# Optimization experiments

Measured on AMD Instinct MI355X. Metric: run time of the kernel, lower is better.

The kernel has to match this reference:

```python
import jax, jax.numpy as jnp
import numpy as np


def _rotate_half(x):
    half = x.shape[-1] // 2
    x1, x2 = x[..., :half], x[..., half:]
    return jnp.concatenate([-x2, x1], axis=-1)


def setup_inputs() -> dict:
    key = jax.random.key(0)
    ks = jax.random.split(key, 7)
    B, T, D, H, Hd = 4, 2048, 1024, 16, 64
    x = jax.random.normal(ks[0], (B, T, D), dtype=jnp.float32)
    # RoPE tables (realistic: built from inv freqs)
    inv_freq = 1.0 / (10000.0 ** (jnp.arange(0, Hd, 2, dtype=jnp.float32) / Hd))
    pos = jnp.arange(T, dtype=jnp.float32)
    freqs = pos[:, None] * inv_freq[None, :]            # (T, Hd/2)
    emb = jnp.concatenate([freqs, freqs], axis=-1)       # (T, Hd)
    cos, sin = jnp.cos(emb), jnp.sin(emb)
    s = 1.0 / np.sqrt(D)
    w_q = jax.random.normal(ks[1], (D, D), dtype=jnp.float32) * s
    w_k = jax.random.normal(ks[2], (D, D), dtype=jnp.float32) * s
    w_v = jax.random.normal(ks[3], (D, D), dtype=jnp.float32) * s
    w_o = jax.random.normal(ks[4], (D, D), dtype=jnp.float32) * s
    return {"x": x, "cos": cos, "sin": sin, "w_q": w_q, "w_k": w_k, "w_v": w_v, "w_o": w_o}


def reference(x, cos, sin, w_q, w_k, w_v, w_o):
    B, T, D = x.shape
    H = 16
    Hd = D // H
    scale = Hd ** -0.5
    # nn.Linear(bias=False): y = x @ W.T
    q = (x @ w_q.T).reshape(B, T, H, Hd).transpose(0, 2, 1, 3)  # (B,H,T,Hd)
    k = (x @ w_k.T).reshape(B, T, H, Hd).transpose(0, 2, 1, 3)
    v = (x @ w_v.T).reshape(B, T, H, Hd).transpose(0, 2, 1, 3)
    c = cos[None, None, :, :]
    s = sin[None, None, :, :]
    q = q * c + _rotate_half(q) * s
    k = k * c + _rotate_half(k) * s
    scores = jnp.einsum('bhqd,bhkd->bhqk', q, k) * scale  # (B,H,T,T)
    causal = jnp.tril(jnp.ones((T, T), dtype=bool))
    scores = jnp.where(causal[None, None], scores, -jnp.inf)
    weights = jax.nn.softmax(scores, axis=-1)
    out = jnp.einsum('bhqk,bhkd->bhqd', weights, v)
    out = out.transpose(0, 2, 1, 3).reshape(B, T, D)
    return out @ w_o.T
```

## Files before the change

kernel.cpp:

```cpp
#include <hip/hip_runtime.h>
#include <stdint.h>

typedef __attribute__((ext_vector_type(8))) __bf16 bf16x8;
typedef __attribute__((ext_vector_type(4))) float floatx4;


__device__ __forceinline__ unsigned short f2bf(float f) {
    unsigned int u = __float_as_uint(f);
    u += 0x7FFFu + ((u >> 16) & 1u);
    return (unsigned short)(u >> 16);
}
__device__ __forceinline__ unsigned int pack2bf(float lo, float hi) {
    return (unsigned int)f2bf(lo) | ((unsigned int)f2bf(hi) << 16);
}
__device__ __forceinline__ unsigned int packtrunc(float lo, float hi) {
    return __builtin_amdgcn_perm(__float_as_uint(hi), __float_as_uint(lo), 0x07060302u);
}

__device__ __forceinline__ void gl_lds16(const void* g, void* l) {
    __builtin_amdgcn_global_load_lds(
        (const __attribute__((address_space(1))) void*)g,
        (__attribute__((address_space(3))) void*)l, 16, 0, 0);
}


__global__ void cvt_all(const float* __restrict__ x,  const float* __restrict__ wq,
                        const float* __restrict__ wk, const float* __restrict__ wv,
                        const float* __restrict__ wo,
                        unsigned short* __restrict__ xb,  unsigned short* __restrict__ wqb,
                        unsigned short* __restrict__ wkb, unsigned short* __restrict__ wvb,
                        unsigned short* __restrict__ wob) {
    int i = blockIdx.x * blockDim.x + threadIdx.x;
    const float* in; unsigned short* out; int idx;
    if (i < 2097152) { in = x; out = xb; idx = i; }
    else {
        int j = i - 2097152; int wsel = j >> 18; idx = j & 262143;
        in  = (wsel == 0) ? wq  : (wsel == 1) ? wk  : (wsel == 2) ? wv  : wo;
        out = (wsel == 0) ? wqb : (wsel == 1) ? wkb : (wsel == 2) ? wvb : wob;
    }
    float4 v = ((const float4*)in)[idx];
    ushort4 o;
    o.x = f2bf(v.x); o.y = f2bf(v.y); o.z = f2bf(v.z); o.w = f2bf(v.w);
    ((ushort4*)out)[idx] = o;
}

__global__ __launch_bounds__(256, 2)
void gemm_qkv(const unsigned short* __restrict__ A,
              const unsigned short* __restrict__ Wq,
              const unsigned short* __restrict__ Wk,
              const unsigned short* __restrict__ Wv,
              const float* __restrict__ cosp,
              const float* __restrict__ sinp,
              unsigned short* __restrict__ outq,
              unsigned short* __restrict__ outk,
              unsigned short* __restrict__ outvt)
{
    constexpr int K = 1024;
    __shared__ __align__(16) unsigned short As[128 * 32];
    __shared__ __align__(16) unsigned short Bs[128 * 32];

    const int t    = threadIdx.x;
    const int w    = t >> 6;
    const int lane = t & 63;
    const int c    = lane & 15;
    const int quad = lane >> 4;
    const int wr   = w >> 1, wc = w & 1;

    const int m0    = blockIdx.x * 128;
    const int which = blockIdx.y >> 3;
    const int n0    = (blockIdx.y & 7) * 128;
    const unsigned short* W = (which == 0) ? Wq : (which == 1) ? Wk : Wv;
    const bool vmode = (which == 2);

    const int srow = t >> 2;
    const int scol = (t & 3) * 8;
    const unsigned short* ga0 = A + (size_t)(m0 + srow) * K + scol;
    const unsigned short* ga1 = A + (size_t)(m0 + srow + 64) * K + scol;
    const unsigned short* gb0 = W + (size_t)(n0 + srow) * K + scol;
    const unsigned short* gb1 = W + (size_t)(n0 + srow + 64) * K + scol;
    void* lA0 = (char*)As + t * 16;
    void* lA1 = (char*)As + 4096 + t * 16;
    void* lB0 = (char*)Bs + t * 16;
    void* lB1 = (char*)Bs + 4096 + t * 16;

    floatx4 acc[4][4] = {};

    const int arow = wr * 64;
    const int brow = wc * 64;

    for (int k0 = 0; k0 < K; k0 += 32) {
        __syncthreads();
        gl_lds16(ga0 + k0, lA0);
        gl_lds16(ga1 + k0, lA1);
        gl_lds16(gb0 + k0, lB0);
        gl_lds16(gb1 + k0, lB1);
        __syncthreads();
        bf16x8 af[4], bfr[4];
        #pragma unroll
        for (int mi = 0; mi < 4; mi++)
            af[mi] = *(const bf16x8*)&As[(arow + mi * 16 + c) * 32 + quad * 8];
        #pragma unroll
        for (int ni = 0; ni < 4; ni++)
            bfr[ni] = *(const bf16x8*)&Bs[(brow + ni * 16 + c) * 32 + quad * 8];
        if (vmode) {
            #pragma unroll
            for (int mi = 0; mi < 4; mi++)
                #pragma unroll
                for (int ni = 0; ni < 4; ni++)
                    acc[mi][ni] = __builtin_amdgcn_mfma_f32_16x16x32_bf16(
                        af[mi], bfr[ni], acc[mi][ni], 0, 0, 0);
        } else {
            #pragma unroll
            for (int mi = 0; mi < 4; mi++)
                #pragma unroll
                for (int ni = 0; ni < 4; ni++)
                    acc[mi][ni] = __builtin_amdgcn_mfma_f32_16x16x32_bf16(
                        bfr[ni], af[mi], acc[mi][ni], 0, 0, 0);
        }
    }

    const int hh = (n0 + wc * 64) >> 6;
    if (vmode) {
        #pragma unroll
        for (int mi = 0; mi < 4; mi++) {
            int t0 = m0 + wr * 64 + mi * 16 + quad * 4;
            int b = t0 >> 11, tt0 = t0 & 2047;
            #pragma unroll
            for (int ni = 0; ni < 4; ni++) {
                int d = ni * 16 + c;
                uint2 pk;
                pk.x = pack2bf(acc[mi][ni][0], acc[mi][ni][1]);
                pk.y = pack2bf(acc[mi][ni][2], acc[mi][ni][3]);
                *(uint2*)&outvt[((size_t)((b * 16 + hh) * 64 + d)) * 2048 + tt0] = pk;
            }
        }
    } else {
        unsigned short* dst = which ? outk : outq;
        const float scale = which ? 1.0f : (0.125f * 1.44269504088896f);
        #pragma unroll
        for (int mi = 0; mi < 4; mi++) {
            int m = m0 + wr * 64 + mi * 16 + c;
            int b = m >> 11, tt = m & 2047;
            size_t obase = ((size_t)(b * 16 + hh) * 2048 + tt) * 64;
            #pragma unroll
            for (int ni = 0; ni < 4; ni++) {
                int d0 = ni * 16 + quad * 4;
                float4 cv = *(const float4*)&cosp[tt * 64 + d0];
                float4 sv = *(const float4*)&sinp[tt * 64 + d0];
                float ca[4] = {cv.x, cv.y, cv.z, cv.w};
                float sa[4] = {sv.x, sv.y, sv.z, sv.w};
                float vq[4];
                #pragma unroll
                for (int r = 0; r < 4; r++) {
                    float pr  = acc[mi][ni ^ 2][r];
                    float rot = (ni & 2) ? pr : -pr;
                    vq[r] = (acc[mi][ni][r] * ca[r] + rot * sa[r]) * scale;
                }
                uint2 pk;
                pk.x = pack2bf(vq[0], vq[1]);
                pk.y = pack2bf(vq[2], vq[3]);
                *(uint2*)&dst[obase + d0] = pk;
            }
        }
    }
}

__global__ __launch_bounds__(256, 2)
void gemm_out(const unsigned short* __restrict__ A,
              const unsigned short* __restrict__ Wo,
              float* __restrict__ outf)
{
    constexpr int K = 1024;
    __shared__ __align__(16) unsigned short As[128 * 32];
    __shared__ __align__(16) unsigned short Bs[128 * 32];

    const int t    = threadIdx.x;
    const int w    = t >> 6;
    const int lane = t & 63;
    const int c    = lane & 15;
    const int quad = lane >> 4;
    const int wr   = w >> 1, wc = w & 1;

    const int m0 = blockIdx.x * 128;
    const int n0 = blockIdx.y * 128;

    const int srow = t >> 2;
    const int scol = (t & 3) * 8;
    const unsigned short* ga0 = A  + (size_t)(m0 + srow) * K + scol;
    const unsigned short* ga1 = A  + (size_t)(m0 + srow + 64) * K + scol;
    const unsigned short* gb0 = Wo + (size_t)(n0 + srow) * K + scol;
    const unsigned short* gb1 = Wo + (size_t)(n0 + srow + 64) * K + scol;
    void* lA0 = (char*)As + t * 16;
    void* lA1 = (char*)As + 4096 + t * 16;
    void* lB0 = (char*)Bs + t * 16;
    void* lB1 = (char*)Bs + 4096 + t * 16;

    floatx4 acc[4][4] = {};

    const int arow = wr * 64;
    const int brow = wc * 64;

    for (int k0 = 0; k0 < K; k0 += 32) {
        __syncthreads();
        gl_lds16(ga0 + k0, lA0);
        gl_lds16(ga1 + k0, lA1);
        gl_lds16(gb0 + k0, lB0);
        gl_lds16(gb1 + k0, lB1);
        __syncthreads();
        bf16x8 af[4], bfr[4];
        #pragma unroll
        for (int mi = 0; mi < 4; mi++)
            af[mi] = *(const bf16x8*)&As[(arow + mi * 16 + c) * 32 + quad * 8];
        #pragma unroll
        for (int ni = 0; ni < 4; ni++)
            bfr[ni] = *(const bf16x8*)&Bs[(brow + ni * 16 + c) * 32 + quad * 8];
        #pragma unroll
        for (int mi = 0; mi < 4; mi++)
            #pragma unroll
            for (int ni = 0; ni < 4; ni++)
                acc[mi][ni] = __builtin_amdgcn_mfma_f32_16x16x32_bf16(
                    bfr[ni], af[mi], acc[mi][ni], 0, 0, 0);
    }

    #pragma unroll
    for (int mi = 0; mi < 4; mi++) {
        int m = m0 + wr * 64 + mi * 16 + c;
        #pragma unroll
        for (int ni = 0; ni < 4; ni++) {
            int n = n0 + wc * 64 + ni * 16 + quad * 4;
            *(floatx4*)&outf[(size_t)m * 1024 + n] = acc[mi][ni];
        }
    }
}

__global__ __launch_bounds__(256)
void flash_attn(const unsigned short* __restrict__ Q,
                const unsigned short* __restrict__ Kg,
                const unsigned short* __restrict__ Vt,
                unsigned short* __restrict__ O)
{
    __shared__ __align__(16) unsigned short Ks[2][64 * 64];
    __shared__ __align__(16) unsigned short Vs[2][64 * 64];
    __shared__ __align__(16) unsigned short Ps[4 * 16 * 64];

    const int t    = threadIdx.x;
    const int w    = t >> 6;
    const int lane = t & 63;
    const int c    = lane & 15;
    const int quad = lane >> 4;

    const int bh = blockIdx.x;
    const int b  = bh >> 4, h = bh & 15;

    const unsigned short* qp = Q  + (size_t)bh * 2048 * 64;
    const unsigned short* kp = Kg + (size_t)bh * 2048 * 64;
    const unsigned short* vp = Vt + (size_t)bh * 64 * 2048;

    const int srow = t >> 3;
    const int sj   = (t & 7) ^ (srow & 7);
    unsigned short* pw = Ps + w * (16 * 64);

    for (int pp = 0; pp < 2; pp++) {
        const int qi = pp ? (31 - (int)blockIdx.y) : (int)blockIdx.y;
        const int q0 = qi * 64;
        const int qb = q0 + w * 16;

        bf16x8 qf[2];
        #pragma unroll
        for (int dc = 0; dc < 2; dc++)
            qf[dc] = *(const bf16x8*)&qp[(size_t)(qb + c) * 64 + dc * 32 + quad * 8];

        floatx4 o[4] = {};
        float lpart = 0.f;

        __syncthreads();
        #pragma unroll
        for (int ch = 0; ch < 2; ch++) {
            int kr = ch * 32 + srow;
            gl_lds16(kp + (size_t)kr * 64 + sj * 8, (char*)&Ks[0][0] + ch * 4096 + t * 16);
            gl_lds16(vp + (size_t)kr * 2048 + sj * 8, (char*)&Vs[0][0] + ch * 4096 + t * 16);
        }

        const int iters = qi + 1;
        for (int it = 0; it < iters; it++) {
            const int cur = it & 1;
            const int kt0 = it * 64;
            __syncthreads();
            if (it + 1 < iters) {
                const int kt1 = kt0 + 64;
                #pragma unroll
                for (int ch = 0; ch < 2; ch++) {
                    int kr = ch * 32 + srow;
                    gl_lds16(kp + (size_t)(kt1 + kr) * 64 + sj * 8,
                             (char*)&Ks[cur ^ 1][0] + ch * 4096 + t * 16);
                    gl_lds16(vp + (size_t)kr * 2048 + kt1 + sj * 8,
                             (char*)&Vs[cur ^ 1][0] + ch * 4096 + t * 16);
                }
            }
            const unsigned short* KsC = &Ks[cur][0];
            const unsigned short* VsC = &Vs[cur][0];

            floatx4 s[4] = {};
            #pragma unroll
            for (int dc = 0; dc < 2; dc++) {
                const int phys = (dc * 4 + quad) ^ (c & 7);
                #pragma unroll
                for (int mt = 0; mt < 4; mt++) {
                    bf16x8 kb = *(const bf16x8*)&KsC[(mt * 16 + c) * 64 + phys * 8];
                    s[mt] = __builtin_amdgcn_mfma_f32_16x16x32_bf16(kb, qf[dc], s[mt], 0, 0, 0);
                }
            }

            if (it == iters - 1) {
                #pragma unroll
                for (int mt = 0; mt < 4; mt++) {
                    int keyb = kt0 + mt * 16 + quad * 4;
                    #pragma unroll
                    for (int r = 0; r < 4; r++)
                        if (keyb + r > qb + c) s[mt][r] = -1e30f;
                }
            }

            uint2 pk[4];
            #pragma unroll
            for (int mt = 0; mt < 4; mt++) {
                float p0 = __builtin_amdgcn_exp2f(s[mt][0]);
                float p1 = __builtin_amdgcn_exp2f(s[mt][1]);
                float p2 = __builtin_amdgcn_exp2f(s[mt][2]);
                float p3 = __builtin_amdgcn_exp2f(s[mt][3]);
                lpart += (p0 + p1) + (p2 + p3);
                pk[mt].x = packtrunc(p0, p1);
                pk[mt].y = packtrunc(p2, p3);
            }

            #pragma unroll
            for (int mt = 0; mt < 4; mt++) {
                int blk = (mt * 2 + (quad >> 1)) ^ (c & 7);
                *(uint2*)&pw[c * 64 + blk * 8 + (quad & 1) * 4] = pk[mt];
            }

            #pragma unroll
            for (int kc = 0; kc < 2; kc++) {
                const int phys = (kc * 4 + quad) ^ (c & 7);
                bf16x8 ap = *(const bf16x8*)&pw[c * 64 + phys * 8];
                #pragma unroll
                for (int ni = 0; ni < 4; ni++) {
                    bf16x8 vb = *(const bf16x8*)&VsC[(ni * 16 + c) * 64 + phys * 8];
                    o[ni] = __builtin_amdgcn_mfma_f32_16x16x32_bf16(ap, vb, o[ni], 0, 0, 0);
                }
            }
        }

        float l = lpart;
        l += __shfl_xor(l, 16);
        l += __shfl_xor(l, 32);
        float li = __builtin_amdgcn_rcpf(l);
        #pragma unroll
        for (int r = 0; r < 4; r++) {
            float linv = __shfl(li, quad * 4 + r);
            int qrow = qb + quad * 4 + r;
            size_t base = ((size_t)(b * 2048 + qrow)) * 1024 + h * 64;
            #pragma unroll
            for (int ni = 0; ni < 4; ni++)
                O[base + ni * 16 + c] = f2bf(o[ni][r] * linv);
        }
    }
}


extern "C" void kernel_launch(void* const* d_in, const int* in_sizes, int n_in,
                              void* d_out, int out_size, void* d_ws, size_t ws_size,
                              hipStream_t stream) {
    const float* x    = (const float*)d_in[0];
    const float* cosp = (const float*)d_in[1];
    const float* sinp = (const float*)d_in[2];
    const float* wq   = (const float*)d_in[3];
    const float* wk   = (const float*)d_in[4];
    const float* wv   = (const float*)d_in[5];
    const float* wo   = (const float*)d_in[6];

    char* ws = (char*)d_ws;
    const size_t MB = 1024 * 1024;
    unsigned short* xb   = (unsigned short*)(ws + 0);
    unsigned short* attn = (unsigned short*)(ws + 0);
    unsigned short* wqb  = (unsigned short*)(ws + 16 * MB);
    unsigned short* wkb  = (unsigned short*)(ws + 18 * MB);
    unsigned short* wvb  = (unsigned short*)(ws + 20 * MB);
    unsigned short* wob  = (unsigned short*)(ws + 22 * MB);
    unsigned short* qbuf = (unsigned short*)(ws + 24 * MB);
    unsigned short* kbuf = (unsigned short*)(ws + 40 * MB);
    unsigned short* vtb  = (unsigned short*)(ws + 56 * MB);

    cvt_all<<<dim3(12288), 256, 0, stream>>>(x, wq, wk, wv, wo,
                                             xb, wqb, wkb, wvb, wob);

    gemm_qkv<<<dim3(64, 24), 256, 0, stream>>>(xb, wqb, wkb, wvb, cosp, sinp,
                                               qbuf, kbuf, vtb);

    flash_attn<<<dim3(64, 16), 256, 0, stream>>>(qbuf, kbuf, vtb, attn);

    gemm_out<<<dim3(64, 8), 256, 0, stream>>>(attn, wob, (float*)d_out);
}
```

Before: 267.1 us.

## Double-buffer LDS tiles in QKV and output projection GEMMs

```diff
diff --git a/kernel.cpp b/kernel.cpp
--- a/kernel.cpp
+++ b/kernel.cpp
@@ -56,8 +56,8 @@
               unsigned short* __restrict__ outvt)
 {
     constexpr int K = 1024;
-    __shared__ __align__(16) unsigned short As[128 * 32];
-    __shared__ __align__(16) unsigned short Bs[128 * 32];
+    __shared__ __align__(16) unsigned short As[2][128 * 32];
+    __shared__ __align__(16) unsigned short Bs[2][128 * 32];
 
     const int t    = threadIdx.x;
     const int w    = t >> 6;
@@ -78,30 +78,33 @@
     const unsigned short* ga1 = A + (size_t)(m0 + srow + 64) * K + scol;
     const unsigned short* gb0 = W + (size_t)(n0 + srow) * K + scol;
     const unsigned short* gb1 = W + (size_t)(n0 + srow + 64) * K + scol;
-    void* lA0 = (char*)As + t * 16;
-    void* lA1 = (char*)As + 4096 + t * 16;
-    void* lB0 = (char*)Bs + t * 16;
-    void* lB1 = (char*)Bs + 4096 + t * 16;
 
     floatx4 acc[4][4] = {};
 
     const int arow = wr * 64;
     const int brow = wc * 64;
 
+    gl_lds16(ga0, (char*)&As[0][0] + t * 16);
+    gl_lds16(ga1, (char*)&As[0][0] + 4096 + t * 16);
+    gl_lds16(gb0, (char*)&Bs[0][0] + t * 16);
+    gl_lds16(gb1, (char*)&Bs[0][0] + 4096 + t * 16);
+
     for (int k0 = 0; k0 < K; k0 += 32) {
+        const int cur = (k0 >> 5) & 1;
         __syncthreads();
-        gl_lds16(ga0 + k0, lA0);
-        gl_lds16(ga1 + k0, lA1);
-        gl_lds16(gb0 + k0, lB0);
-        gl_lds16(gb1 + k0, lB1);
-        __syncthreads();
+        if (k0 + 32 < K) {
+            gl_lds16(ga0 + k0 + 32, (char*)&As[cur ^ 1][0] + t * 16);
+            gl_lds16(ga1 + k0 + 32, (char*)&As[cur ^ 1][0] + 4096 + t * 16);
+            gl_lds16(gb0 + k0 + 32, (char*)&Bs[cur ^ 1][0] + t * 16);
+            gl_lds16(gb1 + k0 + 32, (char*)&Bs[cur ^ 1][0] + 4096 + t * 16);
+        }
         bf16x8 af[4], bfr[4];
         #pragma unroll
         for (int mi = 0; mi < 4; mi++)
-            af[mi] = *(const bf16x8*)&As[(arow + mi * 16 + c) * 32 + quad * 8];
+            af[mi] = *(const bf16x8*)&As[cur][(arow + mi * 16 + c) * 32 + quad * 8];
         #pragma unroll
         for (int ni = 0; ni < 4; ni++)
-            bfr[ni] = *(const bf16x8*)&Bs[(brow + ni * 16 + c) * 32 + quad * 8];
+            bfr[ni] = *(const bf16x8*)&Bs[cur][(brow + ni * 16 + c) * 32 + quad * 8];
         if (vmode) {
             #pragma unroll
             for (int mi = 0; mi < 4; mi++)
@@ -171,8 +174,8 @@
               float* __restrict__ outf)
 {
     constexpr int K = 1024;
-    __shared__ __align__(16) unsigned short As[128 * 32];
-    __shared__ __align__(16) unsigned short Bs[128 * 32];
+    __shared__ __align__(16) unsigned short As[2][128 * 32];
+    __shared__ __align__(16) unsigned short Bs[2][128 * 32];
 
     const int t    = threadIdx.x;
     const int w    = t >> 6;
@@ -190,30 +193,33 @@
     const unsigned short* ga1 = A  + (size_t)(m0 + srow + 64) * K + scol;
     const unsigned short* gb0 = Wo + (size_t)(n0 + srow) * K + scol;
     const unsigned short* gb1 = Wo + (size_t)(n0 + srow + 64) * K + scol;
-    void* lA0 = (char*)As + t * 16;
-    void* lA1 = (char*)As + 4096 + t * 16;
-    void* lB0 = (char*)Bs + t * 16;
-    void* lB1 = (char*)Bs + 4096 + t * 16;
 
     floatx4 acc[4][4] = {};
 
     const int arow = wr * 64;
     const int brow = wc * 64;
 
+    gl_lds16(ga0, (char*)&As[0][0] + t * 16);
+    gl_lds16(ga1, (char*)&As[0][0] + 4096 + t * 16);
+    gl_lds16(gb0, (char*)&Bs[0][0] + t * 16);
+    gl_lds16(gb1, (char*)&Bs[0][0] + 4096 + t * 16);
+
     for (int k0 = 0; k0 < K; k0 += 32) {
+        const int cur = (k0 >> 5) & 1;
         __syncthreads();
-        gl_lds16(ga0 + k0, lA0);
-        gl_lds16(ga1 + k0, lA1);
-        gl_lds16(gb0 + k0, lB0);
-        gl_lds16(gb1 + k0, lB1);
-        __syncthreads();
+        if (k0 + 32 < K) {
+            gl_lds16(ga0 + k0 + 32, (char*)&As[cur ^ 1][0] + t * 16);
+            gl_lds16(ga1 + k0 + 32, (char*)&As[cur ^ 1][0] + 4096 + t * 16);
+            gl_lds16(gb0 + k0 + 32, (char*)&Bs[cur ^ 1][0] + t * 16);
+            gl_lds16(gb1 + k0 + 32, (char*)&Bs[cur ^ 1][0] + 4096 + t * 16);
+        }
         bf16x8 af[4], bfr[4];
         #pragma unroll
         for (int mi = 0; mi < 4; mi++)
-            af[mi] = *(const bf16x8*)&As[(arow + mi * 16 + c) * 32 + quad * 8];
+            af[mi] = *(const bf16x8*)&As[cur][(arow + mi * 16 + c) * 32 + quad * 8];
         #pragma unroll
         for (int ni = 0; ni < 4; ni++)
-            bfr[ni] = *(const bf16x8*)&Bs[(brow + ni * 16 + c) * 32 + quad * 8];
+            bfr[ni] = *(const bf16x8*)&Bs[cur][(brow + ni * 16 + c) * 32 + quad * 8];
         #pragma unroll
         for (int mi = 0; mi < 4; mi++)
             #pragma unroll
```

Measured after the change: 277.4 us. 3.8% more time.
